# Performance work log

Measured on AMD Instinct MI355X. Metric: run time of the kernel, lower is better.

## Reference

```python
import jax, jax.numpy as jnp
import numpy as np

OUT = 3      # pooled output size (fmap_size//4 = 14//4 = 3)
RATIO = 2    # roi_align sampling ratio (fixed; torchvision adaptive ratio for 14/3 bins is 2)
P = 20       # num_persons


def _bilinear(fm, y, x):
    # fm: [C,H,W]; y,x broadcastable coordinate grids. torchvision aligned=False semantics.
    C, H, W = fm.shape
    y, x = jnp.broadcast_arrays(y, x)
    valid = (y > -1.0) & (y < H) & (x > -1.0) & (x < W)
    y = jnp.clip(y, 0.0, H - 1.0)
    x = jnp.clip(x, 0.0, W - 1.0)
    y0 = jnp.floor(y).astype(jnp.int32)
    x0 = jnp.floor(x).astype(jnp.int32)
    y1 = jnp.minimum(y0 + 1, H - 1)
    x1 = jnp.minimum(x0 + 1, W - 1)
    ly = y - y0
    lx = x - x0
    hy = 1.0 - ly
    hx = 1.0 - lx
    v00 = fm[:, y0, x0]
    v01 = fm[:, y0, x1]
    v10 = fm[:, y1, x0]
    v11 = fm[:, y1, x1]
    val = hy * hx * v00 + hy * lx * v01 + ly * hx * v10 + ly * lx * v11
    return jnp.where(valid, val, 0.0)  # [C, ...]


def _roi_align_one(fm, box):
    # fm: [C,H,W], box: [4] = (x1,y1,x2,y2) in feature-map coords -> [C,OUT,OUT]
    x1, y1, x2, y2 = box
    bw = (x2 - x1) / OUT
    bh = (y2 - y1) / OUT
    off = (jnp.arange(OUT * RATIO, dtype=fm.dtype) + 0.5) / RATIO  # bin-unit offsets
    xs = x1 + off * bw
    ys = y1 + off * bh
    vals = _bilinear(fm, ys[:, None], xs[None, :])  # [C, OUT*RATIO, OUT*RATIO]
    C = fm.shape[0]
    return vals.reshape(C, OUT, RATIO, OUT, RATIO).mean(axis=(2, 4))


def setup_inputs() -> dict:
    key = jax.random.key(0)
    ks = jax.random.split(key, 8)
    B, N, NB, C, FS = 128, 8, 27, 1024, 14
    fmap = jax.random.normal(ks[0], (B, C, FS, FS), jnp.float32)
    # boxes in feature-map coordinates with x1<x2, y1<y2
    lo = jax.random.uniform(ks[1], (B, N, 2), jnp.float32) * 10.0
    ext = 2.0 + jax.random.uniform(ks[2], (B, N, 2), jnp.float32) * 4.0
    hi = jnp.minimum(lo + ext, float(FS))
    boxes = jnp.concatenate([lo, hi], axis=-1)  # [B,N,4] (x1,y1,x2,y2)
    # unique person ids per frame (scatter target indices)
    pids = jax.vmap(lambda k: jax.random.permutation(k, P)[:N])(jax.random.split(ks[3], B)).astype(jnp.int32)
    w1 = jax.random.normal(ks[4], (512, C), jnp.float32) * 0.02
    w2 = jax.random.normal(ks[5], (256, 512), jnp.float32) * 0.05
    fc1_w = jax.random.normal(ks[6], (1024, 256 * OUT * OUT), jnp.float32) * 0.02
    fc1_b = jnp.zeros((1024,), jnp.float32)
    fc2_w = jax.random.normal(ks[7], (27, 1024), jnp.float32) * 0.02
    fc2_b = jnp.zeros((27,), jnp.float32)
    return {"fmap": fmap, "boxes": boxes, "pids": pids, "w1": w1, "w2": w2,
            "fc1_w": fc1_w, "fc1_b": fc1_b, "fc2_w": fc2_w, "fc2_b": fc2_b}


def _forward(fmap, boxes, pids, w1, w2, fc1_w, fc1_b, fc2_w, fc2_b):
    B, N = boxes.shape[:2]
    # per-image, per-box ROI align: [B,N,C,3,3]
    roi = jax.vmap(jax.vmap(_roi_align_one, in_axes=(None, 0)), in_axes=(0, 0))(fmap, boxes)
    # behavior_conv: two bias-free 1x1 convs (no nonlinearity between)
    h = jnp.einsum('bnchw,oc->bnohw', roi, w1)
    h = jnp.einsum('bnchw,oc->bnohw', h, w2)  # [B,N,256,3,3]
    feat = h.reshape(B, N, -1)                # [B,N,2304]
    bidx = jnp.broadcast_to(jnp.arange(B)[:, None], (B, N))
    # scatter into behavior_tensor keyed by person id (unique pids per frame -> well-defined)
    bt = jnp.zeros((B, P, feat.shape[-1]), feat.dtype).at[bidx, pids].set(feat)
    mean_b = bt.mean(axis=0)                  # [P,2304] mean over batch
    cur = bt[bidx, pids]                      # [B,N,2304]
    diff = mean_b[pids] - cur
    # behavior_fc (dropout is identity at inference)
    h1 = jax.nn.relu(jnp.einsum('bnd,hd->bnh', diff, fc1_w) + fc1_b)
    return jnp.einsum('bnh,oh->bno', h1, fc2_w) + fc2_b  # [B,N,num_behaviors]


def reference(fmap, boxes, pids, w1, w2, fc1_w, fc1_b, fc2_w, fc2_b):
    # fmap is detached and roi_align runs under no_grad in the original
    return _forward(jax.lax.stop_gradient(fmap), jax.lax.stop_gradient(boxes), pids,
                    w1, w2, fc1_w, fc1_b, fc2_w, fc2_b)
```

## Files before the change

### kernel.cpp

```cpp
#include <hip/hip_runtime.h>
#include <hip/hip_bf16.h>
#include <cstddef>
#include <cstdint>

#define B_   128
#define N_   8
#define C_   1024
#define FS_  14
#define POS_ 196
#define P_   20
#define HWC_ 9
#define CMID_ 256
#define FEATD_ 2304
#define H1_  1024
#define O_   27
#define PROWS_ (B_*N_*HWC_)

typedef __attribute__((ext_vector_type(8))) short bf16x8;
typedef __attribute__((ext_vector_type(4))) float f32x4;

__device__ __forceinline__ void gld16(const void* g, void* l) {
    __builtin_amdgcn_global_load_lds(
        (const __attribute__((address_space(1))) unsigned int*)g,
        (__attribute__((address_space(3))) unsigned int*)l, 16, 0, 0);
}

__global__ __launch_bounds__(256) void wcombine_split_kernel(
    const float* __restrict__ w1,
    const float* __restrict__ w2,
    float* __restrict__ wpart)
{
    const int tid = threadIdx.x;
    const int tx = tid & 15, ty = tid >> 4;
    const int c0 = blockIdx.x * 64;
    const int o0 = blockIdx.y * 64;
    const int kb = blockIdx.z * 64;
    __shared__ __align__(16) float As[16][68];
    __shared__ __align__(16) float Bs[16][68];
    float acc[4][4] = {};
    for (int k0 = kb; k0 < kb + 64; k0 += 16) {
        for (int i = tid; i < 64 * 16; i += 256) {
            int k = i & 15, m = i >> 4;
            As[k][m] = w2[(size_t)(o0 + m) * 512 + k0 + k];
        }
        for (int i = tid; i < 64 * 16; i += 256) {
            int n = i & 63, k = i >> 6;
            Bs[k][n] = w1[(size_t)(k0 + k) * 1024 + c0 + n];
        }
        __syncthreads();
        #pragma unroll
        for (int k = 0; k < 16; ++k) {
            float4 a = *(const float4*)&As[k][ty * 4];
            float4 b = *(const float4*)&Bs[k][tx * 4];
            float av[4] = {a.x, a.y, a.z, a.w};
            float bv[4] = {b.x, b.y, b.z, b.w};
            #pragma unroll
            for (int i = 0; i < 4; ++i)
                #pragma unroll
                for (int j = 0; j < 4; ++j)
                    acc[i][j] += av[i] * bv[j];
        }
        __syncthreads();
    }
    float* dst = wpart + (size_t)blockIdx.z * (256 * 1024);
    for (int i = 0; i < 4; ++i) {
        float4 v = make_float4(acc[i][0], acc[i][1], acc[i][2], acc[i][3]);
        *(float4*)&dst[(size_t)(o0 + ty * 4 + i) * 1024 + c0 + tx * 4] = v;
    }
}

__global__ __launch_bounds__(256) void wc_reduce_kernel(
    const float* __restrict__ wpart, __hip_bfloat16* __restrict__ Wc)
{
    int idx = blockIdx.x * 256 + threadIdx.x;
    float s = 0.f;
    #pragma unroll
    for (int z = 0; z < 8; ++z) s += wpart[(size_t)z * (256 * 1024) + idx];
    Wc[idx] = __float2bfloat16(s);
}

#define CCH_   32
#define LSTR_  197
#define NSAMP_ 288
__global__ __launch_bounds__(256, 5) void roipool_kernel(
    const float* __restrict__ fmap,
    const float* __restrict__ boxes,
    __hip_bfloat16* __restrict__ pooled)
{
    const int b  = blockIdx.y;
    const int c0 = blockIdx.x * CCH_;
    const int tid = threadIdx.x;
    __shared__ float Ls[CCH_ * LSTR_];
    __shared__ int   Tpos[NSAMP_];
    __shared__ __align__(16) float Tw[NSAMP_ * 4];

    const float* src = fmap + ((size_t)b * C_ + c0) * POS_;
    for (int i = tid; i < CCH_ * 49; i += 256) {
        int c = i / 49, ch = i - c * 49;
        float4 v = *(const float4*)(src + (size_t)c * POS_ + ch * 4);
        float* dst = &Ls[c * LSTR_ + ch * 4];
        dst[0] = v.x; dst[1] = v.y; dst[2] = v.z; dst[3] = v.w;
    }

    for (int s = tid; s < NSAMP_; s += 256) {
        int n = s / 36, rem = s - n * 36;
        int cell = rem >> 2, tap = rem & 3;
        int chh = cell / 3, cww = cell % 3;
        int si = tap >> 1, sj = tap & 1;
        const float* bx = boxes + ((size_t)b * N_ + n) * 4;
        float x1 = bx[0], y1 = bx[1], x2 = bx[2], y2 = bx[3];
        float bw = (x2 - x1) * (1.0f / 3.0f);
        float bh = (y2 - y1) * (1.0f / 3.0f);
        float yy = y1 + ((float)(2 * chh + si) + 0.5f) * 0.5f * bh;
        float xx = x1 + ((float)(2 * cww + sj) + 0.5f) * 0.5f * bw;
        bool valid = (yy > -1.0f) && (yy < (float)FS_) &&
                     (xx > -1.0f) && (xx < (float)FS_);
        float y = fminf(fmaxf(yy, 0.0f), (float)(FS_ - 1));
        float x = fminf(fmaxf(xx, 0.0f), (float)(FS_ - 1));
        int y0 = (int)floorf(y);
        int x0 = (int)floorf(x);
        int y1i = min(y0 + 1, FS_ - 1);
        int x1i = min(x0 + 1, FS_ - 1);
        float ly = y - (float)y0, lx = x - (float)x0;
        float hy = 1.0f - ly,     hx = 1.0f - lx;
        float q = valid ? 0.25f : 0.0f;
        int p00 = (y0 * FS_ + x0) * 4;
        int dxb = (x1i - x0) * 4;
        int dyb = (y1i - y0) * (FS_ * 4);
        Tpos[s] = p00 | (dxb << 12) | (dyb << 16);
        Tw[s * 4 + 0] = hy * hx * q;
        Tw[s * 4 + 1] = hy * lx * q;
        Tw[s * 4 + 2] = ly * hx * q;
        Tw[s * 4 + 3] = ly * lx * q;
    }
    __syncthreads();

    const int cl = tid & 31;
    const int n  = tid >> 5;
    const char* lsb = (const char*)&Ls[cl * LSTR_];
    __hip_bfloat16* prow = pooled + (size_t)((b * N_ + n) * HWC_) * C_ + c0 + cl;

    #pragma unroll
    for (int cell = 0; cell < 9; ++cell) {
        float acc = 0.0f;
        const int sbase = n * 36 + cell * 4;
        #pragma unroll
        for (int tap = 0; tap < 4; ++tap) {
            int pk = Tpos[sbase + tap];
            float4 w = *(const float4*)&Tw[(sbase + tap) * 4];
            int p00 = pk & 0xFFF;
            int dxb = (pk >> 12) & 0xF;
            int dyb = pk >> 16;
            float v00 = *(const float*)(lsb + p00);
            float v01 = *(const float*)(lsb + p00 + dxb);
            float v10 = *(const float*)(lsb + p00 + dyb);
            float v11 = *(const float*)(lsb + p00 + dyb + dxb);
            acc = fmaf(w.x, v00, acc);
            acc = fmaf(w.y, v01, acc);
            acc = fmaf(w.z, v10, acc);
            acc = fmaf(w.w, v11, acc);
        }
        prow[(size_t)cell * C_] = __float2bfloat16(acc);
    }
}

__global__ __launch_bounds__(256, 4) void pooledgemm_kernel(
    const __hip_bfloat16* __restrict__ A,
    const __hip_bfloat16* __restrict__ Bm,
    float* __restrict__ Cout)
{
    const int tid = threadIdx.x;
    const int wave = tid >> 6, lane = tid & 63;
    const int r0 = blockIdx.y * 64, n0 = blockIdx.x * 64;
    const int wm = (wave >> 1) * 32, wn = (wave & 1) * 32;
    const int m16 = lane & 15, quad = lane >> 4;
    const int K = C_;
    __shared__ __align__(16) __hip_bfloat16 As[64 * 64];
    __shared__ __align__(16) __hip_bfloat16 Bs[64 * 64];

    f32x4 acc[2][2];
    #pragma unroll
    for (int i = 0; i < 2; ++i)
        #pragma unroll
        for (int j = 0; j < 2; ++j)
            acc[i][j] = (f32x4){0.f, 0.f, 0.f, 0.f};

    const int qa = wave * 64 + lane;
    const int ms0 = qa >> 3, cs0 = (qa & 7) ^ (ms0 & 7);
    const int qb1 = qa + 256;
    const int ms1 = qb1 >> 3, cs1 = (qb1 & 7) ^ (ms1 & 7);
    const size_t rA0 = (size_t)(r0 + ms0) * K + cs0 * 8;
    const size_t rA1 = (size_t)(r0 + ms1) * K + cs1 * 8;
    const size_t rB0 = (size_t)(n0 + ms0) * K + cs0 * 8;
    const size_t rB1 = (size_t)(n0 + ms1) * K + cs1 * 8;

    for (int k0 = 0; k0 < K; k0 += 64) {
        gld16(A  + rA0 + k0, &As[wave * 512]);
        gld16(Bm + rB0 + k0, &Bs[wave * 512]);
        gld16(A  + rA1 + k0, &As[2048 + wave * 512]);
        gld16(Bm + rB1 + k0, &Bs[2048 + wave * 512]);
        __syncthreads();
        #pragma unroll
        for (int ks = 0; ks < 2; ++ks) {
            bf16x8 af[2], bfv[2];
            #pragma unroll
            for (int t = 0; t < 2; ++t) {
                int m = wm + t * 16 + m16;
                int cp = (ks * 4 + quad) ^ (m & 7);
                af[t] = *(const bf16x8*)&As[(m * 8 + cp) * 8];
                int n = wn + t * 16 + m16;
                int cq = (ks * 4 + quad) ^ (n & 7);
                bfv[t] = *(const bf16x8*)&Bs[(n * 8 + cq) * 8];
            }
            #pragma unroll
            for (int i = 0; i < 2; ++i)
                #pragma unroll
                for (int j = 0; j < 2; ++j)
                    acc[i][j] = __builtin_amdgcn_mfma_f32_16x16x32_bf16(
                        af[i], bfv[j], acc[i][j], 0, 0, 0);
        }
        __syncthreads();
    }

    #pragma unroll
    for (int i = 0; i < 2; ++i) {
        #pragma unroll
        for (int j = 0; j < 2; ++j) {
            int col = n0 + wn + j * 16 + m16;
            int rbase = r0 + wm + i * 16 + quad * 4;
            #pragma unroll
            for (int g = 0; g < 4; ++g)
                Cout[(size_t)(rbase + g) * 256 + col] = acc[i][j][g];
        }
    }
}

__global__ __launch_bounds__(256, 4) void fc1_gemm_kernel(
    const __hip_bfloat16* __restrict__ A,
    const __hip_bfloat16* __restrict__ Bm,
    const float* __restrict__ bias,
    float* __restrict__ C)
{
    const int tid = threadIdx.x;
    const int wave = tid >> 6, lane = tid & 63;
    const int r0 = blockIdx.y * 32, n0 = blockIdx.x * 64;
    const int wm = (wave >> 1) * 16, wn = (wave & 1) * 32;
    const int m16 = lane & 15, quad = lane >> 4;
    const int K = FEATD_;
    __shared__ __align__(16) __hip_bfloat16 As[32 * 64];
    __shared__ __align__(16) __hip_bfloat16 Bs[64 * 64];

    f32x4 acc[2];
    acc[0] = (f32x4){0.f, 0.f, 0.f, 0.f};
    acc[1] = (f32x4){0.f, 0.f, 0.f, 0.f};

    const int qa = wave * 64 + lane;
    const int msA = qa >> 3, csA = (qa & 7) ^ (msA & 7);
    const int qb1 = qa + 256;
    const int msB1 = qb1 >> 3, csB1 = (qb1 & 7) ^ (msB1 & 7);
    const size_t rA  = (size_t)(r0 + msA)  * K + csA  * 8;
    const size_t rB0 = (size_t)(n0 + msA)  * K + csA  * 8;
    const size_t rB1 = (size_t)(n0 + msB1) * K + csB1 * 8;

    for (int k0 = 0; k0 < K; k0 += 64) {
        gld16(A  + rA  + k0, &As[wave * 512]);
        gld16(Bm + rB0 + k0, &Bs[wave * 512]);
        gld16(Bm + rB1 + k0, &Bs[2048 + wave * 512]);
        __syncthreads();
        #pragma unroll
        for (int ks = 0; ks < 2; ++ks) {
            bf16x8 af, bfv[2];
            int m = wm + m16;
            int cp = (ks * 4 + quad) ^ (m & 7);
            af = *(const bf16x8*)&As[(m * 8 + cp) * 8];
            #pragma unroll
            for (int t = 0; t < 2; ++t) {
                int n = wn + t * 16 + m16;
                int cq = (ks * 4 + quad) ^ (n & 7);
                bfv[t] = *(const bf16x8*)&Bs[(n * 8 + cq) * 8];
            }
            #pragma unroll
            for (int j = 0; j < 2; ++j)
                acc[j] = __builtin_amdgcn_mfma_f32_16x16x32_bf16(
                    af, bfv[j], acc[j], 0, 0, 0);
        }
        __syncthreads();
    }

    #pragma unroll
    for (int j = 0; j < 2; ++j) {
        int col = n0 + wn + j * 16 + m16;
        int rbase = r0 + wm + quad * 4;
        float bv = bias[col];
        #pragma unroll
        for (int g = 0; g < 4; ++g) {
            int r = rbase + g;
            float v = acc[j][g] + bv;
            C[(size_t)r * H1_ + col] = v > 0.f ? v : 0.f;
        }
    }
}

__global__ __launch_bounds__(256) void fc1w_perm_kernel(
    const float* __restrict__ src, __hip_bfloat16* __restrict__ dst)
{
    int h = blockIdx.x;
    int tid = threadIdx.x;
    __shared__ float buf[FEATD_];
    const float* s = src + (size_t)h * FEATD_;
    #pragma unroll
    for (int it = 0; it < 9; ++it)
        buf[it * 256 + tid] = s[it * 256 + tid];
    __syncthreads();
    __hip_bfloat16* d = dst + (size_t)h * FEATD_;
    #pragma unroll
    for (int it = 0; it < 9; ++it) {
        int dd = it * 256 + tid;
        d[dd] = __float2bfloat16(buf[tid * HWC_ + it]);
    }
}

__global__ __launch_bounds__(64) void invmap_kernel(
    const int* __restrict__ pids, int* __restrict__ inv)
{
    int b = blockIdx.x;
    int p = threadIdx.x;
    if (p < P_) {
        int v = -1;
        for (int n = 0; n < N_; ++n)
            if (pids[b * N_ + n] == p) v = n;
        inv[b * P_ + p] = v;
    }
}

__global__ __launch_bounds__(256) void meandiff_kernel(
    const float* __restrict__ feat, const int* __restrict__ inv,
    __hip_bfloat16* __restrict__ diff)
{
    int p = blockIdx.x;
    int d = blockIdx.y * 256 + threadIdx.x;
    float acc = 0.0f;
    #pragma unroll 4
    for (int b = 0; b < B_; ++b) {
        int n = inv[b * P_ + p];
        if (n >= 0) acc += feat[(size_t)(b * N_ + n) * FEATD_ + d];
    }
    float mean = acc * (1.0f / (float)B_);
    #pragma unroll 4
    for (int b = 0; b < B_; ++b) {
        int n = inv[b * P_ + p];
        if (n >= 0) {
            size_t r = (size_t)(b * N_ + n);
            diff[r * FEATD_ + d] = __float2bfloat16(mean - feat[r * FEATD_ + d]);
        }
    }
}

__global__ __launch_bounds__(256) void fc2_kernel(
    const float* __restrict__ h1, const float* __restrict__ fc2_w,
    const float* __restrict__ fc2_b, float* __restrict__ out)
{
    int bn = blockIdx.x;
    int tid = threadIdx.x;
    __shared__ __align__(16) float row[H1_];
    __shared__ float partial[32][8];
    ((float4*)row)[tid] = ((const float4*)(h1 + (size_t)bn * H1_))[tid];
    __syncthreads();
    int o = tid >> 3, part = tid & 7;
    float acc = 0.0f;
    if (o < O_) {
        const float* wrow = fc2_w + (size_t)o * H1_ + part * 128;
        const float* hrow = row + part * 128;
        #pragma unroll 4
        for (int j = 0; j < 128; ++j) acc += hrow[j] * wrow[j];
    }
    partial[o][part] = acc;
    __syncthreads();
    if (part == 0 && o < O_) {
        float s = fc2_b[o];
        #pragma unroll
        for (int p = 0; p < 8; ++p) s += partial[o][p];
        out[(size_t)bn * O_ + o] = s;
    }
}

extern "C" void kernel_launch(void* const* d_in, const int* in_sizes, int n_in,
                              void* d_out, int out_size, void* d_ws, size_t ws_size,
                              hipStream_t stream) {
    const float* fmap  = (const float*)d_in[0];
    const float* boxes = (const float*)d_in[1];
    const int*   pids  = (const int*)  d_in[2];
    const float* w1    = (const float*)d_in[3];
    const float* w2    = (const float*)d_in[4];
    const float* fc1_w = (const float*)d_in[5];
    const float* fc1_b = (const float*)d_in[6];
    const float* fc2_w = (const float*)d_in[7];
    const float* fc2_b = (const float*)d_in[8];
    float* out = (float*)d_out;

    char* wsb = (char*)d_ws;
    __hip_bfloat16* Wc     = (__hip_bfloat16*)wsb;
    __hip_bfloat16* pooled = Wc + 256 * 1024;
    __hip_bfloat16* fc1wp  = pooled + (size_t)PROWS_ * C_;
    __hip_bfloat16* diffp  = fc1wp + (size_t)H1_ * FEATD_;
    float* feat   = (float*)(diffp + (size_t)H1_ * FEATD_);
    float* mean_b = feat + (size_t)(B_ * N_) * FEATD_;
    float* h1     = mean_b + (size_t)P_ * FEATD_;
    int*   inv    = (int*)(h1 + (size_t)(B_ * N_) * H1_);
    float* wpart  = (float*)(inv + 128 * P_ + 64);

    hipLaunchKernelGGL(wcombine_split_kernel, dim3(16, 4, 8), dim3(256), 0, stream,
                       w1, w2, wpart);
    hipLaunchKernelGGL(wc_reduce_kernel, dim3(1024), dim3(256), 0, stream,
                       wpart, Wc);
    hipLaunchKernelGGL(roipool_kernel, dim3(C_ / CCH_, 128), dim3(256), 0, stream,
                       fmap, boxes, pooled);
    hipLaunchKernelGGL(pooledgemm_kernel, dim3(4, 144), dim3(256), 0, stream,
                       pooled, Wc, feat);
    hipLaunchKernelGGL(fc1w_perm_kernel, dim3(1024), dim3(256), 0, stream,
                       fc1_w, fc1wp);
    hipLaunchKernelGGL(invmap_kernel, dim3(128), dim3(64), 0, stream,
                       pids, inv);
    hipLaunchKernelGGL(meandiff_kernel, dim3(20, 9), dim3(256), 0, stream,
                       feat, inv, diffp);
    hipLaunchKernelGGL(fc1_gemm_kernel, dim3(16, 32), dim3(256), 0, stream,
                       diffp, fc1wp, fc1_b, h1);
    hipLaunchKernelGGL(fc2_kernel, dim3(1024), dim3(256), 0, stream,
                       h1, fc2_w, fc2_b, out);
}
```

Before: 299.0 us.

## Recast ROI-align pooling as a bf16 MFMA matmul with an interpolation matrix

The ROI pooling kernel now builds a 72x196 bilinear interpolation weight matrix in shared memory, one row per box-cell, and stores the feature-map tile as bf16. It then computes the pooled output with 16x16x32 bf16 MFMA instructions instead of per-thread scalar gathers from LDS. The channel chunk grows to 64 and occupancy bounds change to match. This trades the scattered LDS gathers and FMAs for dense matrix-core work, at the cost of bf16 rounding of both the input features and the interpolation weights, which are also accumulated in bf16.

```diff
diff --git a/kernel.cpp b/kernel.cpp
--- a/kernel.cpp
+++ b/kernel.cpp
@@ -79,10 +79,12 @@
     Wc[idx] = __float2bfloat16(s);
 }
 
-#define CCH_   32
-#define LSTR_  197
-#define NSAMP_ 288
-__global__ __launch_bounds__(256, 5) void roipool_kernel(
+#define CCH_   64
+#define SSTR_  232
+#define AROWS_ 72
+#define AOFF_  (AROWS_ * SSTR_)
+struct bf4s { __hip_bfloat162 lo, hi; };
+__global__ __launch_bounds__(256, 2) void roipool_kernel(
     const float* __restrict__ fmap,
     const float* __restrict__ boxes,
     __hip_bfloat16* __restrict__ pooled)
@@ -90,77 +92,114 @@
     const int b  = blockIdx.y;
     const int c0 = blockIdx.x * CCH_;
     const int tid = threadIdx.x;
-    __shared__ float Ls[CCH_ * LSTR_];
-    __shared__ int   Tpos[NSAMP_];
-    __shared__ __align__(16) float Tw[NSAMP_ * 4];
-
+    __shared__ __align__(16) __hip_bfloat16 Ls[(AROWS_ + CCH_) * SSTR_];
+
+    float4 vbuf[13];
     const float* src = fmap + ((size_t)b * C_ + c0) * POS_;
-    for (int i = tid; i < CCH_ * 49; i += 256) {
-        int c = i / 49, ch = i - c * 49;
-        float4 v = *(const float4*)(src + (size_t)c * POS_ + ch * 4);
-        float* dst = &Ls[c * LSTR_ + ch * 4];
-        dst[0] = v.x; dst[1] = v.y; dst[2] = v.z; dst[3] = v.w;
-    }
-
-    for (int s = tid; s < NSAMP_; s += 256) {
-        int n = s / 36, rem = s - n * 36;
-        int cell = rem >> 2, tap = rem & 3;
-        int chh = cell / 3, cww = cell % 3;
-        int si = tap >> 1, sj = tap & 1;
-        const float* bx = boxes + ((size_t)b * N_ + n) * 4;
-        float x1 = bx[0], y1 = bx[1], x2 = bx[2], y2 = bx[3];
+    #pragma unroll
+    for (int it = 0; it < 13; ++it) {
+        int i = tid + it * 256;
+        if (i < CCH_ * 49) {
+            int c = i / 49, ch = i - c * 49;
+            vbuf[it] = *(const float4*)(src + (size_t)c * POS_ + ch * 4);
+        }
+    }
+    {
+        const uint4 z = {0, 0, 0, 0};
+        #pragma unroll
+        for (int it = 0; it < 9; ++it) {
+            int i = tid + it * 256;
+            if (i < 2088) *(uint4*)((char*)Ls + i * 16) = z;
+        }
+    }
+    #pragma unroll
+    for (int it = 0; it < 13; ++it) {
+        int i = tid + it * 256;
+        if (i < CCH_ * 49) {
+            int c = i / 49, ch = i - c * 49;
+            float4 v = vbuf[it];
+            bf4s t;
+            t.lo.x = __float2bfloat16(v.x); t.lo.y = __float2bfloat16(v.y);
+            t.hi.x = __float2bfloat16(v.z); t.hi.y = __float2bfloat16(v.w);
+            *(bf4s*)&Ls[AOFF_ + c * SSTR_ + ch * 4] = t;
+        }
+    }
+    {
+        #pragma unroll
+        for (int it = 0; it < 5; ++it) {
+            int i = tid + it * 256;
+            if (i < CCH_ * 18) {
+                int r = i / 18, kd = i - r * 18;
+                *(unsigned int*)&Ls[AOFF_ + r * SSTR_ + 196 + kd * 2] = 0;
+            }
+        }
+    }
+    __syncthreads();
+
+    if (tid < AROWS_) {
+        const int m = tid;
+        const int n = m / 9, cell = m - n * 9;
+        const int chh = cell / 3, cww = cell % 3;
+        float4 bx = *(const float4*)(boxes + ((size_t)b * N_ + n) * 4);
+        float x1 = bx.x, y1 = bx.y, x2 = bx.z, y2 = bx.w;
         float bw = (x2 - x1) * (1.0f / 3.0f);
         float bh = (y2 - y1) * (1.0f / 3.0f);
-        float yy = y1 + ((float)(2 * chh + si) + 0.5f) * 0.5f * bh;
-        float xx = x1 + ((float)(2 * cww + sj) + 0.5f) * 0.5f * bw;
-        bool valid = (yy > -1.0f) && (yy < (float)FS_) &&
-                     (xx > -1.0f) && (xx < (float)FS_);
-        float y = fminf(fmaxf(yy, 0.0f), (float)(FS_ - 1));
-        float x = fminf(fmaxf(xx, 0.0f), (float)(FS_ - 1));
-        int y0 = (int)floorf(y);
-        int x0 = (int)floorf(x);
-        int y1i = min(y0 + 1, FS_ - 1);
-        int x1i = min(x0 + 1, FS_ - 1);
-        float ly = y - (float)y0, lx = x - (float)x0;
-        float hy = 1.0f - ly,     hx = 1.0f - lx;
-        float q = valid ? 0.25f : 0.0f;
-        int p00 = (y0 * FS_ + x0) * 4;
-        int dxb = (x1i - x0) * 4;
-        int dyb = (y1i - y0) * (FS_ * 4);
-        Tpos[s] = p00 | (dxb << 12) | (dyb << 16);
-        Tw[s * 4 + 0] = hy * hx * q;
-        Tw[s * 4 + 1] = hy * lx * q;
-        Tw[s * 4 + 2] = ly * hx * q;
-        Tw[s * 4 + 3] = ly * lx * q;
+        __hip_bfloat16* row = &Ls[m * SSTR_];
+        #pragma unroll
+        for (int si = 0; si < 2; ++si) {
+            float yy = y1 + ((float)(2 * chh + si) + 0.5f) * 0.5f * bh;
+            #pragma unroll
+            for (int sj = 0; sj < 2; ++sj) {
+                float xx = x1 + ((float)(2 * cww + sj) + 0.5f) * 0.5f * bw;
+                bool valid = (yy > -1.0f) && (yy < (float)FS_) &&
+                             (xx > -1.0f) && (xx < (float)FS_);
+                float y = fminf(fmaxf(yy, 0.0f), (float)(FS_ - 1));
+                float x = fminf(fmaxf(xx, 0.0f), (float)(FS_ - 1));
+                int y0 = (int)floorf(y);
+                int x0 = (int)floorf(x);
+                int y1i = min(y0 + 1, FS_ - 1);
+                int x1i = min(x0 + 1, FS_ - 1);
+                float ly = y - (float)y0, lx = x - (float)x0;
+                float hy = 1.0f - ly,     hx = 1.0f - lx;
+                float q = valid ? 0.25f : 0.0f;
+                int p00 = y0 * FS_ + x0, p01 = y0 * FS_ + x1i;
+                int p10 = y1i * FS_ + x0, p11 = y1i * FS_ + x1i;
+                row[p00] = __float2bfloat16(__bfloat162float(row[p00]) + hy * hx * q);
+                row[p01] = __float2bfloat16(__bfloat162float(row[p01]) + hy * lx * q);
+                row[p10] = __float2bfloat16(__bfloat162float(row[p10]) + ly * hx * q);
+                row[p11] = __float2bfloat16(__bfloat162float(row[p11]) + ly * lx * q);
+            }
+        }
     }
     __syncthreads();
 
-    const int cl = tid & 31;
-    const int n  = tid >> 5;
-    const char* lsb = (const char*)&Ls[cl * LSTR_];
-    __hip_bfloat16* prow = pooled + (size_t)((b * N_ + n) * HWC_) * C_ + c0 + cl;
-
-    #pragma unroll
-    for (int cell = 0; cell < 9; ++cell) {
-        float acc = 0.0f;
-        const int sbase = n * 36 + cell * 4;
-        #pragma unroll
-        for (int tap = 0; tap < 4; ++tap) {
-            int pk = Tpos[sbase + tap];
-            float4 w = *(const float4*)&Tw[(sbase + tap) * 4];
-            int p00 = pk & 0xFFF;
-            int dxb = (pk >> 12) & 0xF;
-            int dyb = pk >> 16;
-            float v00 = *(const float*)(lsb + p00);
-            float v01 = *(const float*)(lsb + p00 + dxb);
-            float v10 = *(const float*)(lsb + p00 + dyb);
-            float v11 = *(const float*)(lsb + p00 + dyb + dxb);
-            acc = fmaf(w.x, v00, acc);
-            acc = fmaf(w.y, v01, acc);
-            acc = fmaf(w.z, v10, acc);
-            acc = fmaf(w.w, v11, acc);
-        }
-        prow[(size_t)cell * C_] = __float2bfloat16(acc);
+    const int wave = tid >> 6, lane = tid & 63;
+    const int m16 = lane & 15, quad = lane >> 4;
+    f32x4 acc[5];
+    #pragma unroll
+    for (int mt = 0; mt < 5; ++mt) acc[mt] = (f32x4){0.f, 0.f, 0.f, 0.f};
+
+    const int nrow = wave * 16 + m16;
+    #pragma unroll
+    for (int kk = 0; kk < 7; ++kk) {
+        bf16x8 bfv = *(const bf16x8*)&Ls[AOFF_ + nrow * SSTR_ + kk * 32 + quad * 8];
+        #pragma unroll
+        for (int mt = 0; mt < 5; ++mt) {
+            bf16x8 af = *(const bf16x8*)&Ls[(mt * 16 + m16) * SSTR_ + kk * 32 + quad * 8];
+            acc[mt] = __builtin_amdgcn_mfma_f32_16x16x32_bf16(af, bfv, acc[mt], 0, 0, 0);
+        }
+    }
+
+    const int col = c0 + wave * 16 + m16;
+    #pragma unroll
+    for (int mt = 0; mt < 5; ++mt) {
+        #pragma unroll
+        for (int g = 0; g < 4; ++g) {
+            int row = mt * 16 + quad * 4 + g;
+            if (row < AROWS_)
+                pooled[(size_t)(b * AROWS_ + row) * C_ + col] =
+                    __float2bfloat16(acc[mt][g]);
+        }
     }
 }
 
```

Measured after the change: 296.4 us. No clear change (-0.9%).
